# Performance work log

Hardware: AMD Instinct MI355X
Metric: run time of the kernel (lower is better)

Reference implementation:

```python
import jax, jax.numpy as jnp
import numpy as np
from jax import lax

B, T, V, E, H, K = 64, 512, 50002, 300, 256, 11
START, STOP = 9, 10


def _lstm_dir(x, w_ih, w_hh, b, reverse):
    """Single-direction LSTM. x: [B,T,D]; w_ih: [4H,D]; w_hh: [4H,H]; b: [4H]."""
    xw = jnp.einsum('btd,gd->btg', x, w_ih) + b  # precompute input projections [B,T,4H]
    h0 = jnp.zeros((x.shape[0], w_hh.shape[1]), x.dtype)

    def step(carry, xt):
        h, c = carry
        g = xt + h @ w_hh.T                      # [B,4H], gate order i,f,g,o (PyTorch)
        i, f, gg, o = jnp.split(g, 4, axis=-1)
        c = jax.nn.sigmoid(f) * c + jax.nn.sigmoid(i) * jnp.tanh(gg)
        h = jax.nn.sigmoid(o) * jnp.tanh(c)
        return (h, c), h

    _, hs = lax.scan(step, (h0, h0), jnp.swapaxes(xw, 0, 1), reverse=reverse)
    return jnp.swapaxes(hs, 0, 1)  # [B,T,H]


def _bilstm_feats(sentence, emb, fc_w, fc_b,
                  w_ih_l0f, w_hh_l0f, b_l0f, w_ih_l0b, w_hh_l0b, b_l0b,
                  w_ih_l1f, w_hh_l1f, b_l1f, w_ih_l1b, w_hh_l1b, b_l1b):
    x = emb[sentence]  # [B,T,E] (frozen embedding lookup)
    h0 = jnp.concatenate([
        _lstm_dir(x, w_ih_l0f, w_hh_l0f, b_l0f, False),
        _lstm_dir(x, w_ih_l0b, w_hh_l0b, b_l0b, True)], axis=-1)  # [B,T,2H]
    h1 = jnp.concatenate([
        _lstm_dir(h0, w_ih_l1f, w_hh_l1f, b_l1f, False),
        _lstm_dir(h0, w_ih_l1b, w_hh_l1b, b_l1b, True)], axis=-1)  # [B,T,2H]
    return h1 @ fc_w.T + fc_b  # emission scores [B,T,K] (dropout = identity in eval)


def _viterbi(feats, transitions):
    """feats: [B,T,K]; transitions[to, from]: [K,K]. Returns (path_score [B,1], path [B,T])."""
    Bs = feats.shape[0]
    init = jnp.full((Bs, K), -1000.0, feats.dtype).at[:, START].set(0.0)

    def step(fv, feat_t):
        scores = fv[:, None, :] + transitions[None, :, :]  # [B, next, prev]
        best_prev = jnp.argmax(scores, axis=2)             # [B,K]
        vit = jnp.max(scores, axis=2)                      # [B,K]
        return vit + feat_t, best_prev

    fv, bptrs = lax.scan(step, init, jnp.swapaxes(feats, 0, 1))  # bptrs: [T,B,K]
    terminal = fv + transitions[STOP]                             # [B,K]
    path_score = jnp.max(terminal, axis=1, keepdims=True)         # [B,1]
    last_tag = jnp.argmax(terminal, axis=1)                       # [B]

    def back(tag, bp):
        prev = jnp.take_along_axis(bp, tag[:, None], axis=1)[:, 0]
        return prev, prev

    _, prev_tags = lax.scan(back, last_tag, bptrs, reverse=True)  # prev_tags[t] = tag at t-1
    path = jnp.concatenate([prev_tags[1:], last_tag[None]], axis=0)  # [T,B]; drop START
    return path_score, jnp.swapaxes(path, 0, 1)


def setup_inputs() -> dict:
    key = jax.random.key(0)
    ks = jax.random.split(key, 24)
    s = 1.0 / np.sqrt(H)
    inp = {
        'sentence': jax.random.randint(ks[0], (B, T), 0, V, dtype=jnp.int32),
        'batch_lengths': jnp.full((B,), T, dtype=jnp.int32),
        'emb': jax.random.normal(ks[1], (V, E), jnp.float32) * 0.1,
        'fc_w': jax.random.normal(ks[2], (K, 2 * H), jnp.float32) * s,
        'fc_b': jnp.zeros((K,), jnp.float32),
    }
    trans = jax.random.normal(ks[3], (K, K), jnp.float32)
    inp['transitions'] = trans.at[START, :].set(-100000.0).at[:, STOP].set(-100000.0)
    i = 4
    for layer, din in ((0, E), (1, 2 * H)):
        for d in ('f', 'b'):
            inp[f'w_ih_l{layer}{d}'] = jax.random.normal(ks[i], (4 * H, din), jnp.float32) * s
            inp[f'w_hh_l{layer}{d}'] = jax.random.normal(ks[i + 1], (4 * H, H), jnp.float32) * s
            inp[f'b_l{layer}{d}'] = jax.random.normal(ks[i + 2], (4 * H,), jnp.float32) * s
            i += 3
    return inp


def reference(sentence, batch_lengths, emb, fc_w, fc_b, transitions,
              w_ih_l0f, w_hh_l0f, b_l0f, w_ih_l0b, w_hh_l0b, b_l0b,
              w_ih_l1f, w_hh_l1f, b_l1f, w_ih_l1b, w_hh_l1b, b_l1b):
    feats = _bilstm_feats(sentence, emb, fc_w, fc_b,
                          w_ih_l0f, w_hh_l0f, b_l0f, w_ih_l0b, w_hh_l0b, b_l0b,
                          w_ih_l1f, w_hh_l1f, b_l1f, w_ih_l1b, w_hh_l1b, b_l1b)
    score, path = _viterbi(feats, transitions)
    return score, path
```

## Files before the change

kernel.cpp:

```cpp
#include <hip/hip_runtime.h>
#include <cstddef>
#include <cstdint>
#include <math.h>


__device__ __forceinline__ float sigmf_(float x){ return 1.0f/(1.0f+expf(-x)); }

__global__ void k_zero(float* __restrict__ p, int n){
  for (int i = blockIdx.x*blockDim.x + threadIdx.x; i < n; i += gridDim.x*blockDim.x) p[i] = 0.f;
}

__global__ void k_gather(const int* __restrict__ sent, const float* __restrict__ emb,
                         float4* __restrict__ X, int b0, int t0, int logT, int Tm1, int total){
  int idx = blockIdx.x*256 + threadIdx.x;
  if (idx >= total) return;
  int m = idx / 76, k4 = idx - m*76;
  int bl = m >> logT, t = m & Tm1;
  float4 v = make_float4(0.f,0.f,0.f,0.f);
  if (k4 < 75) v = ((const float4*)emb)[(size_t)sent[(size_t)(b0+bl)*512 + t0 + t]*75 + k4];
  X[idx] = v;
}

__global__ void k_prepw(const float* __restrict__ w, float* __restrict__ wT, int din, int dinPad){
  int total = dinPad*1024;
  for (int idx = blockIdx.x*blockDim.x + threadIdx.x; idx < total; idx += gridDim.x*blockDim.x){
    int k = idx >> 10, n = idx & 1023;
    wT[idx] = (k < din) ? w[n*din + k] : 0.f;
  }
}

__global__ __launch_bounds__(256) void k_gemm2(
    const float* __restrict__ A0, const float* __restrict__ A1, int lda, int kTiles,
    int aBstride, int sOff0, int sOff1, int logT, int Tm1,
    const float* __restrict__ B0, const float* __restrict__ B1,
    const float* __restrict__ bias0, const float* __restrict__ bias1,
    float* __restrict__ C0, float* __restrict__ C1){
  __shared__ float As[16][132];
  __shared__ float Bs[16][132];
  const int z = blockIdx.z;
  const float* A   = z ? A1 : A0;
  const float* Bm  = z ? B1 : B0;
  const float* bias= z ? bias1 : bias0;
  float* Cc        = z ? C1 : C0;
  const int sOff   = z ? sOff1 : sOff0;
  const int t  = threadIdx.x;
  const int tx = t & 15, ty = t >> 4;
  const int m0 = blockIdx.y * 128, n0 = blockIdx.x * 128;
  const int arow = t >> 2, ak = (t & 3) * 4;
  const int brow = t >> 5, bc = (t & 31) * 4;
  const int gm0 = m0 + arow, gm1 = m0 + arow + 64;
  const size_t r0 = (size_t)(gm0 >> logT)*aBstride + sOff + (gm0 & Tm1);
  const size_t r1 = (size_t)(gm1 >> logT)*aBstride + sOff + (gm1 & Tm1);
  float acc[8][8] = {};
  for (int kt = 0; kt < kTiles; ++kt){
    const int kb = kt * 16;
    float4 a0 = *(const float4*)(A + r0*lda + kb + ak);
    float4 a1 = *(const float4*)(A + r1*lda + kb + ak);
    float4 b0 = *(const float4*)(Bm + (size_t)(kb+brow)*1024 + n0 + bc);
    float4 b1 = *(const float4*)(Bm + (size_t)(kb+brow+8)*1024 + n0 + bc);
    __syncthreads();
    As[ak+0][arow] = a0.x; As[ak+1][arow] = a0.y; As[ak+2][arow] = a0.z; As[ak+3][arow] = a0.w;
    As[ak+0][arow+64] = a1.x; As[ak+1][arow+64] = a1.y; As[ak+2][arow+64] = a1.z; As[ak+3][arow+64] = a1.w;
    *(float4*)&Bs[brow  ][bc] = b0;
    *(float4*)&Bs[brow+8][bc] = b1;
    __syncthreads();
    #pragma unroll
    for (int k = 0; k < 16; ++k){
      float av[8], bv[8];
      *(float4*)&av[0] = *(const float4*)&As[k][ty*8];
      *(float4*)&av[4] = *(const float4*)&As[k][ty*8+4];
      *(float4*)&bv[0] = *(const float4*)&Bs[k][tx*8];
      *(float4*)&bv[4] = *(const float4*)&Bs[k][tx*8+4];
      #pragma unroll
      for (int i = 0; i < 8; ++i)
        #pragma unroll
        for (int jj = 0; jj < 8; ++jj)
          acc[i][jj] = fmaf(av[i], bv[jj], acc[i][jj]);
    }
  }
  float bvals[8];
  *(float4*)&bvals[0] = *(const float4*)(bias + n0 + tx*8);
  *(float4*)&bvals[4] = *(const float4*)(bias + n0 + tx*8 + 4);
  float* Cp = Cc + (size_t)(m0 + ty*8)*1024 + n0 + tx*8;
  #pragma unroll
  for (int i = 0; i < 8; ++i){
    float4 o0 = make_float4(acc[i][0]+bvals[0], acc[i][1]+bvals[1], acc[i][2]+bvals[2], acc[i][3]+bvals[3]);
    float4 o1 = make_float4(acc[i][4]+bvals[4], acc[i][5]+bvals[5], acc[i][6]+bvals[6], acc[i][7]+bvals[7]);
    *(float4*)(Cp + (size_t)i*1024)     = o0;
    *(float4*)(Cp + (size_t)i*1024 + 4) = o1;
  }
}

__global__ __launch_bounds__(512) __attribute__((amdgpu_waves_per_eu(2, 2)))
void k_lstm2s(
    const float* __restrict__ xwF, const float* __restrict__ xwB,
    const float* __restrict__ whhf, const float* __restrict__ whhb,
    float* __restrict__ hout, int hBstride, int tOffF, int tOffB,
    int T, int epoch,
    float* __restrict__ hx, int* __restrict__ flags,
    float* __restrict__ hsave, float* __restrict__ csave)
{
  __shared__ float hfull[256];
  __shared__ float gls[512];
  __shared__ float wtail[512*66];
  const int blk = blockIdx.x;
  const int hh = (blk >> 3) & 1;
  const int chain = (blk & 7) | ((blk >> 4) << 3);
  const int b_local = chain >> 1;
  const int dir = chain & 1;
  const int t = threadIdx.x;
  const int gateK = t >> 7, i0 = t & 127;
  float4 wL[24], wR[24];
  {
    const float* whh = dir ? whhb : whhf;
    const float* base = whh + (size_t)(gateK*256 + hh*128 + i0)*256;
    const float* a = base + hh*128;
    const float* b = base + (1-hh)*128;
    #pragma unroll
    for (int q = 0; q < 24; ++q){ wL[q] = *(const float4*)(a + q*4); wR[q] = *(const float4*)(b + q*4); }
    for (int q = 24; q < 32; ++q){
      #pragma unroll
      for (int e = 0; e < 4; ++e){
        wtail[t*66 + (q-24)*4 + e]      = a[q*4 + e];
        wtail[t*66 + 32 + (q-24)*4 + e] = b[q*4 + e];
      }
    }
  }
  if (t < 256) hfull[t] = hsave[chain*256 + t];
  float c = (t < 128) ? csave[chain*256 + hh*128 + t] : 0.f;
  __syncthreads();
  const int xcol = gateK*256 + hh*128 + i0;
  const float* xb = (dir ? xwB : xwF) + (size_t)b_local*T*1024 + xcol;
  float* hxme        = hx + (size_t)(chain*2 + hh)*256;
  const float* hxpt  = hx + (size_t)(chain*2 + (1-hh))*256;
  int* flg  = flags + (chain*2 + hh)*16;
  int* flgp = flags + (chain*2 + (1-hh))*16;
  const int tOff = dir ? tOffB : tOffF;
  float* hob = hout + (size_t)b_local*hBstride + dir*256 + hh*128;
  const float* wtb = &wtail[t*66];
  const float4* hL4 = ((const float4*)hfull) + hh*32;
  const float4* hR4 = ((const float4*)hfull) + (1-hh)*32;
  float xg = xb[(size_t)(dir ? (T-1) : 0)*1024];
  float2 hrem = make_float2(0.f, 0.f);
  for (int s = 0; s < T; ++s){
    const int tt = dir ? (T-1-s) : s;
    float xn = 0.f;
    if (s < T-1) xn = xb[(size_t)(dir ? (T-2-s) : (s+1))*1024];
    if (s > 0 && t < 64){
      hfull[(1-hh)*128 + 2*t]     = hrem.x;
      hfull[(1-hh)*128 + 2*t + 1] = hrem.y;
    }
    float pa = 0.f;
    #pragma unroll
    for (int q = 0; q < 24; ++q){
      float4 hv = hL4[q];
      pa = fmaf(wL[q].x, hv.x, pa);
      pa = fmaf(wL[q].y, hv.y, pa);
      pa = fmaf(wL[q].z, hv.z, pa);
      pa = fmaf(wL[q].w, hv.w, pa);
    }
    #pragma unroll
    for (int q = 24; q < 32; ++q){
      float4 hv = hL4[q];
      const int o = (q-24)*4;
      pa = fmaf(wtb[o+0], hv.x, pa);
      pa = fmaf(wtb[o+1], hv.y, pa);
      pa = fmaf(wtb[o+2], hv.z, pa);
      pa = fmaf(wtb[o+3], hv.w, pa);
    }
    __syncthreads();
    float pb = 0.f;
    #pragma unroll
    for (int q = 0; q < 24; ++q){
      float4 hv = hR4[q];
      pb = fmaf(wR[q].x, hv.x, pb);
      pb = fmaf(wR[q].y, hv.y, pb);
      pb = fmaf(wR[q].z, hv.z, pb);
      pb = fmaf(wR[q].w, hv.w, pb);
    }
    #pragma unroll
    for (int q = 24; q < 32; ++q){
      float4 hv = hR4[q];
      const int o = (q-24)*4;
      pb = fmaf(wtb[32+o+0], hv.x, pb);
      pb = fmaf(wtb[32+o+1], hv.y, pb);
      pb = fmaf(wtb[32+o+2], hv.z, pb);
      pb = fmaf(wtb[32+o+3], hv.w, pb);
    }
    float acc = (pa + pb) + xg;
    float act = (gateK == 2) ? tanhf(acc) : sigmf_(acc);
    gls[t] = act;
    __syncthreads();
    float hval = 0.f;
    if (t < 128){
      c = gls[128 + t]*c + gls[t]*gls[256 + t];
      hval = gls[384 + t]*tanhf(c);
      hfull[hh*128 + t] = hval;
      __hip_atomic_store(&hxme[(s & 1)*128 + t], hval,
                         __ATOMIC_RELAXED, __HIP_MEMORY_SCOPE_AGENT);
    }
    __syncthreads();
    if (t == 0)
      __hip_atomic_store(flg, epoch + s + 1, __ATOMIC_RELAXED, __HIP_MEMORY_SCOPE_AGENT);
    if (t < 128) hob[(size_t)(tOff + tt)*512 + t] = hval;
    if (s < T-1){
      if (t == 0){
        int lim = 0;
        while (__hip_atomic_load(flgp, __ATOMIC_RELAXED, __HIP_MEMORY_SCOPE_AGENT) < epoch + s + 1
               && ++lim < (1<<20)) {}
      }
      if (t < 64){
        union { unsigned long long u; float2 f; } uu;
        uu.u = __hip_atomic_load((const unsigned long long*)(hxpt + (s & 1)*128 + 2*t),
                                 __ATOMIC_RELAXED, __HIP_MEMORY_SCOPE_AGENT);
        hrem = uu.f;
      }
    }
    xg = xn;
  }
  if (t < 128){
    hsave[chain*256 + hh*128 + t] = hfull[hh*128 + t];
    csave[chain*256 + hh*128 + t] = c;
  }
}

__global__ __launch_bounds__(256) void k_feats_half(
    const float* __restrict__ h1s, const float* __restrict__ fcw, const float* __restrict__ fcb,
    float* __restrict__ feats, int b0, int logT, int Tm1, int tG0, int dir){
  int wv = threadIdx.x >> 6, lane = threadIdx.x & 63;
  int m = blockIdx.x*4 + wv;
  const float4* row = (const float4*)(h1s + (size_t)m*512 + dir*256);
  float4 rv = row[lane];
  int bl = m >> logT, tl = m & Tm1;
  size_t fbase = ((size_t)(b0 + bl)*512 + tG0 + tl)*11;
  #pragma unroll
  for (int n = 0; n < 11; ++n){
    const float4* wr = (const float4*)(fcw + n*512 + dir*256);
    float4 w4 = wr[lane];
    float p = rv.x*w4.x + rv.y*w4.y + rv.z*w4.z + rv.w*w4.w;
    #pragma unroll
    for (int off = 32; off > 0; off >>= 1) p += __shfl_down(p, off, 64);
    if (lane == 0){
      float add = (dir == 0) ? (p + fcb[n]) : p;
      feats[fbase + n] += add;
    }
  }
}

__global__ __launch_bounds__(256) void k_viterbi(const float* __restrict__ feats,
                        const float* __restrict__ trans, float* __restrict__ out){
  __shared__ unsigned char bp[4][512][12];
  const int wave = threadIdx.x >> 6, lane = threadIdx.x & 63;
  const int b = blockIdx.x*4 + wave;
  const int j = lane;
  float tr[11];
  float fv;
  if (j < 11){
    #pragma unroll
    for (int p = 0; p < 11; ++p) tr[p] = trans[j*11 + p];
    fv = (j == 9) ? 0.f : -1000.f;
  } else {
    #pragma unroll
    for (int p = 0; p < 11; ++p) tr[p] = -1e30f;
    fv = -1e30f;
  }
  const float* fb = feats + ((size_t)b*512)*11 + j;
  float f0 = (j < 11) ? fb[0*11] : 0.f;
  float f1 = (j < 11) ? fb[1*11] : 0.f;
  float f2 = (j < 11) ? fb[2*11] : 0.f;
  float f3 = (j < 11) ? fb[3*11] : 0.f;
#define VSTEP(TT, FREG) {                                            \
    float best = -1e38f; int bestp = 0;                              \
    _Pragma("unroll")                                                \
    for (int p = 0; p < 11; ++p){                                    \
      float v = __shfl(fv, p, 64) + tr[p];                           \
      if (v > best){ best = v; bestp = p; }                          \
    }                                                                \
    fv = best + FREG;                                                \
    if (j < 11) bp[wave][TT][j] = (unsigned char)bestp; }
  for (int t = 0; t < 512; t += 4){
    VSTEP(t+0, f0); f0 = (j < 11 && t+4 < 512) ? fb[(size_t)(t+4)*11] : 0.f;
    VSTEP(t+1, f1); f1 = (j < 11 && t+5 < 512) ? fb[(size_t)(t+5)*11] : 0.f;
    VSTEP(t+2, f2); f2 = (j < 11 && t+6 < 512) ? fb[(size_t)(t+6)*11] : 0.f;
    VSTEP(t+3, f3); f3 = (j < 11 && t+7 < 512) ? fb[(size_t)(t+7)*11] : 0.f;
  }
#undef VSTEP
  float term = (j < 11) ? fv + trans[10*11 + j] : -1e38f;
  float best = -1e38f; int bestp = 0;
  #pragma unroll
  for (int p = 0; p < 11; ++p){
    float v = __shfl(term, p, 64);
    if (v > best){ best = v; bestp = p; }
  }
  if (lane == 0){
    out[b] = best;
    float* path = out + 64 + (size_t)b*512;
    int cur = bestp;
    path[511] = (float)cur;
    for (int t = 511; t >= 1; --t){
      cur = bp[wave][t][cur];
      path[t-1] = (float)cur;
    }
  }
}

extern "C" void kernel_launch(void* const* d_in, const int* in_sizes, int n_in,
                              void* d_out, int out_size, void* d_ws, size_t ws_size,
                              hipStream_t stream){
  const int*   sent  = (const int*)d_in[0];
  const float* emb   = (const float*)d_in[2];
  const float* fcw   = (const float*)d_in[3];
  const float* fcb   = (const float*)d_in[4];
  const float* trans = (const float*)d_in[5];
  const float* wih0f = (const float*)d_in[6];
  const float* whh0f = (const float*)d_in[7];
  const float* b0f   = (const float*)d_in[8];
  const float* wih0b = (const float*)d_in[9];
  const float* whh0b = (const float*)d_in[10];
  const float* b0b   = (const float*)d_in[11];
  const float* wih1f = (const float*)d_in[12];
  const float* whh1f = (const float*)d_in[13];
  const float* b1f   = (const float*)d_in[14];
  const float* wih1b = (const float*)d_in[15];
  const float* whh1b = (const float*)d_in[16];
  const float* b1b   = (const float*)d_in[17];

  float* ws = (float*)d_ws;
  const size_t o_wT0f = 0;
  const size_t o_wT0b = o_wT0f + 311296;
  const size_t o_wT1f = o_wT0b + 311296;
  const size_t o_wT1b = o_wT1f + 524288;
  const size_t o_hx   = o_wT1b + 524288;
  const size_t o_flag = o_hx   + 65536;
  const size_t o_hs   = o_flag + 4096;
  const size_t o_cs   = o_hs   + 32768;
  const size_t o_feat = o_cs   + 32768;
  const size_t o_var  = o_feat + 360448;
  float* wT0f = ws + o_wT0f;
  float* wT0b = ws + o_wT0b;
  float* wT1f = ws + o_wT1f;
  float* wT1b = ws + o_wT1b;
  float* hx    = ws + o_hx;
  int*   flags = (int*)(ws + o_flag);
  float* hsave = ws + o_hs;
  float* csave = ws + o_cs;
  float* feats = ws + o_feat;

  int C = 8, T = 32, logT = 5;
  {
    const int cc[9]  = {64, 64, 64, 32, 32, 16, 16, 8, 8};
    const int tt[9]  = {64, 32, 16, 32, 16, 32, 16, 64, 32};
    const int lt[9]  = { 6,  5,  4,  5,  4,  5,  4,  6,  5};
    for (int i = 0; i < 9; ++i){
      size_t need = (o_var + (size_t)cc[i]*tt[i]*2656 + (size_t)cc[i]*262144)*4;
      if (need <= ws_size){ C = cc[i]; T = tt[i]; logT = lt[i]; break; }
    }
  }
  const int Tm1 = T - 1, S = 512 / T;
  float* XF  = ws + o_var;
  float* XB  = XF + (size_t)C*T*304;
  float* xwF = XB + (size_t)C*T*304;
  float* xwB = xwF + (size_t)C*T*1024;
  float* h0  = xwB + (size_t)C*T*1024;
  float* h1s = XF;

  hipLaunchKernelGGL(k_prepw, dim3(512), dim3(256), 0, stream, wih0f, wT0f, 300, 304);
  hipLaunchKernelGGL(k_prepw, dim3(512), dim3(256), 0, stream, wih0b, wT0b, 300, 304);
  hipLaunchKernelGGL(k_prepw, dim3(512), dim3(256), 0, stream, wih1f, wT1f, 512, 512);
  hipLaunchKernelGGL(k_prepw, dim3(512), dim3(256), 0, stream, wih1b, wT1b, 512, 512);
  hipLaunchKernelGGL(k_zero,  dim3(512), dim3(256), 0, stream, feats, 360448);

  for (int b0 = 0; b0 < 64; b0 += C){
    for (int layer = 0; layer < 2; ++layer){
      hipLaunchKernelGGL(k_zero, dim3(256), dim3(256), 0, stream, ws + o_hx, 65536 + 4096 + 65536);
      const float* whF = layer ? whh1f : whh0f;
      const float* whB = layer ? whh1b : whh0b;
      for (int sl = 0; sl < S; ++sl){
        const int sF = sl, sB = S - 1 - sl;
        const int M = C*T;
        if (layer == 0){
          int total = C*T*76;
          hipLaunchKernelGGL(k_gather, dim3((total+255)/256), dim3(256), 0, stream,
                             sent, emb, (float4*)XF, b0, sF*T, logT, Tm1, total);
          hipLaunchKernelGGL(k_gather, dim3((total+255)/256), dim3(256), 0, stream,
                             sent, emb, (float4*)XB, b0, sB*T, logT, Tm1, total);
          hipLaunchKernelGGL(k_gemm2, dim3(8, M/128, 2), dim3(256), 0, stream,
                             XF, XB, 304, 19, T, 0, 0, logT, Tm1,
                             wT0f, wT0b, b0f, b0b, xwF, xwB);
        } else {
          hipLaunchKernelGGL(k_gemm2, dim3(8, M/128, 2), dim3(256), 0, stream,
                             h0, h0, 512, 32, 512, sF*T, sB*T, logT, Tm1,
                             wT1f, wT1b, b1f, b1b, xwF, xwB);
        }
        {
          const float *xF = xwF, *xB = xwB, *wF = whF, *wB = whB;
          float* hop = layer ? h1s : h0;
          int hBs  = layer ? T*512 : 512*512;
          int tOF  = layer ? 0 : sF*T;
          int tOB  = layer ? 0 : sB*T;
          int Tk = T, ep = sl*T;
          float *hxp = hx, *hsp = hsave, *csp = csave; int *flp = flags;
          void* args[] = {(void*)&xF, (void*)&xB, (void*)&wF, (void*)&wB,
                          (void*)&hop, (void*)&hBs, (void*)&tOF, (void*)&tOB,
                          (void*)&Tk, (void*)&ep,
                          (void*)&hxp, (void*)&flp, (void*)&hsp, (void*)&csp};
          hipLaunchCooperativeKernel((const void*)k_lstm2s, dim3(C*4), dim3(512), args, 0, stream);
        }
        if (layer == 1){
          hipLaunchKernelGGL(k_feats_half, dim3(C*T/4), dim3(256), 0, stream,
                             h1s, fcw, fcb, feats, b0, logT, Tm1, sF*T, 0);
          hipLaunchKernelGGL(k_feats_half, dim3(C*T/4), dim3(256), 0, stream,
                             h1s, fcw, fcb, feats, b0, logT, Tm1, sB*T, 1);
        }
      }
    }
  }
  hipLaunchKernelGGL(k_viterbi, dim3(16), dim3(256), 0, stream, feats, trans, (float*)d_out);
}
```

Baseline: 5.635 ms.

## Pack epoch tags with h values and move gate combine to wave shuffles

```diff
diff --git a/kernel.cpp b/kernel.cpp
--- a/kernel.cpp
+++ b/kernel.cpp
@@ -5,6 +5,13 @@
 
 
 __device__ __forceinline__ float sigmf_(float x){ return 1.0f/(1.0f+expf(-x)); }
+
+__device__ __forceinline__ void bar_sync(){
+  __builtin_amdgcn_sched_barrier(0);
+  asm volatile("s_waitcnt lgkmcnt(0)" ::: "memory");
+  __builtin_amdgcn_s_barrier();
+  __builtin_amdgcn_sched_barrier(0);
+}
 
 __global__ void k_zero(float* __restrict__ p, int n){
   for (int i = blockIdx.x*blockDim.x + threadIdx.x; i < n; i += gridDim.x*blockDim.x) p[i] = 0.f;
@@ -97,11 +104,10 @@
     const float* __restrict__ whhf, const float* __restrict__ whhb,
     float* __restrict__ hout, int hBstride, int tOffF, int tOffB,
     int T, int epoch,
-    float* __restrict__ hx, int* __restrict__ flags,
+    unsigned long long* __restrict__ hx,
     float* __restrict__ hsave, float* __restrict__ csave)
 {
   __shared__ float hfull[256];
-  __shared__ float gls[512];
   __shared__ float wtail[512*66];
   const int blk = blockIdx.x;
   const int hh = (blk >> 3) & 1;
@@ -109,7 +115,9 @@
   const int b_local = chain >> 1;
   const int dir = chain & 1;
   const int t = threadIdx.x;
-  const int gateK = t >> 7, i0 = t & 127;
+  const int w = t >> 6, l = t & 63;
+  const int gateK = l >> 4;
+  const int i0 = w*16 + (l & 15);
   float4 wL[24], wR[24];
   {
     const float* whh = dir ? whhb : whhf;
@@ -127,29 +135,23 @@
     }
   }
   if (t < 256) hfull[t] = hsave[chain*256 + t];
-  float c = (t < 128) ? csave[chain*256 + hh*128 + t] : 0.f;
+  float c = (l < 16) ? csave[chain*256 + hh*128 + i0] : 0.f;
   __syncthreads();
   const int xcol = gateK*256 + hh*128 + i0;
   const float* xb = (dir ? xwB : xwF) + (size_t)b_local*T*1024 + xcol;
-  float* hxme        = hx + (size_t)(chain*2 + hh)*256;
-  const float* hxpt  = hx + (size_t)(chain*2 + (1-hh))*256;
-  int* flg  = flags + (chain*2 + hh)*16;
-  int* flgp = flags + (chain*2 + (1-hh))*16;
+  unsigned long long* hxme       = hx + (size_t)(chain*2 + hh)*256;
+  const unsigned long long* hxpt = hx + (size_t)(chain*2 + (1-hh))*256;
   const int tOff = dir ? tOffB : tOffF;
   float* hob = hout + (size_t)b_local*hBstride + dir*256 + hh*128;
   const float* wtb = &wtail[t*66];
   const float4* hL4 = ((const float4*)hfull) + hh*32;
   const float4* hR4 = ((const float4*)hfull) + (1-hh)*32;
   float xg = xb[(size_t)(dir ? (T-1) : 0)*1024];
-  float2 hrem = make_float2(0.f, 0.f);
+  float hlast = 0.f;
   for (int s = 0; s < T; ++s){
     const int tt = dir ? (T-1-s) : s;
     float xn = 0.f;
     if (s < T-1) xn = xb[(size_t)(dir ? (T-2-s) : (s+1))*1024];
-    if (s > 0 && t < 64){
-      hfull[(1-hh)*128 + 2*t]     = hrem.x;
-      hfull[(1-hh)*128 + 2*t + 1] = hrem.y;
-    }
     float pa = 0.f;
     #pragma unroll
     for (int q = 0; q < 24; ++q){
@@ -168,7 +170,22 @@
       pa = fmaf(wtb[o+2], hv.z, pa);
       pa = fmaf(wtb[o+3], hv.w, pa);
     }
-    __syncthreads();
+    if (s > 0 && w == 0){
+      const unsigned long long* src = hxpt + (size_t)(((s-1)&1))*128;
+      const unsigned want = (unsigned)(epoch + s);
+      unsigned long long v0 = 0, v1 = 0;
+      bool ok0 = false, ok1 = false;
+      int lim = 0;
+      do {
+        if (!ok0){ v0 = __hip_atomic_load(src + 2*l,     __ATOMIC_RELAXED, __HIP_MEMORY_SCOPE_AGENT);
+                   ok0 = (unsigned)(v0 >> 32) == want; }
+        if (!ok1){ v1 = __hip_atomic_load(src + 2*l + 1, __ATOMIC_RELAXED, __HIP_MEMORY_SCOPE_AGENT);
+                   ok1 = (unsigned)(v1 >> 32) == want; }
+      } while (__any(!(ok0 && ok1)) && ++lim < (1<<20));
+      hfull[(1-hh)*128 + 2*l]     = __uint_as_float((unsigned)v0);
+      hfull[(1-hh)*128 + 2*l + 1] = __uint_as_float((unsigned)v1);
+    }
+    bar_sync();
     float pb = 0.f;
     #pragma unroll
     for (int q = 0; q < 24; ++q){
@@ -189,38 +206,26 @@
     }
     float acc = (pa + pb) + xg;
     float act = (gateK == 2) ? tanhf(acc) : sigmf_(acc);
-    gls[t] = act;
-    __syncthreads();
-    float hval = 0.f;
-    if (t < 128){
-      c = gls[128 + t]*c + gls[t]*gls[256 + t];
-      hval = gls[384 + t]*tanhf(c);
-      hfull[hh*128 + t] = hval;
-      __hip_atomic_store(&hxme[(s & 1)*128 + t], hval,
+    float fg = __shfl(act, (l & 15) + 16, 64);
+    float gg = __shfl(act, (l & 15) + 32, 64);
+    float og = __shfl(act, (l & 15) + 48, 64);
+    if (l < 16){
+      c = fg*c + act*gg;
+      float hval = og*tanhf(c);
+      hlast = hval;
+      hfull[hh*128 + i0] = hval;
+      unsigned long long pk = ((unsigned long long)(unsigned)(epoch + s + 1) << 32)
+                            | (unsigned long long)__float_as_uint(hval);
+      __hip_atomic_store(&hxme[(size_t)(s & 1)*128 + i0], pk,
                          __ATOMIC_RELAXED, __HIP_MEMORY_SCOPE_AGENT);
-    }
-    __syncthreads();
-    if (t == 0)
-      __hip_atomic_store(flg, epoch + s + 1, __ATOMIC_RELAXED, __HIP_MEMORY_SCOPE_AGENT);
-    if (t < 128) hob[(size_t)(tOff + tt)*512 + t] = hval;
-    if (s < T-1){
-      if (t == 0){
-        int lim = 0;
-        while (__hip_atomic_load(flgp, __ATOMIC_RELAXED, __HIP_MEMORY_SCOPE_AGENT) < epoch + s + 1
-               && ++lim < (1<<20)) {}
-      }
-      if (t < 64){
-        union { unsigned long long u; float2 f; } uu;
-        uu.u = __hip_atomic_load((const unsigned long long*)(hxpt + (s & 1)*128 + 2*t),
-                                 __ATOMIC_RELAXED, __HIP_MEMORY_SCOPE_AGENT);
-        hrem = uu.f;
-      }
-    }
+      hob[(size_t)(tOff + tt)*512 + i0] = hval;
+    }
+    bar_sync();
     xg = xn;
   }
-  if (t < 128){
-    hsave[chain*256 + hh*128 + t] = hfull[hh*128 + t];
-    csave[chain*256 + hh*128 + t] = c;
+  if (l < 16){
+    hsave[chain*256 + hh*128 + i0] = hlast;
+    csave[chain*256 + hh*128 + i0] = c;
   }
 }
 
@@ -331,8 +336,7 @@
   const size_t o_wT1f = o_wT0b + 311296;
   const size_t o_wT1b = o_wT1f + 524288;
   const size_t o_hx   = o_wT1b + 524288;
-  const size_t o_flag = o_hx   + 65536;
-  const size_t o_hs   = o_flag + 4096;
+  const size_t o_hs   = o_hx   + 131072;
   const size_t o_cs   = o_hs   + 32768;
   const size_t o_feat = o_cs   + 32768;
   const size_t o_var  = o_feat + 360448;
@@ -340,18 +344,17 @@
   float* wT0b = ws + o_wT0b;
   float* wT1f = ws + o_wT1f;
   float* wT1b = ws + o_wT1b;
-  float* hx    = ws + o_hx;
-  int*   flags = (int*)(ws + o_flag);
+  unsigned long long* hx = (unsigned long long*)(ws + o_hx);
   float* hsave = ws + o_hs;
   float* csave = ws + o_cs;
   float* feats = ws + o_feat;
 
   int C = 8, T = 32, logT = 5;
   {
-    const int cc[9]  = {64, 64, 64, 32, 32, 16, 16, 8, 8};
-    const int tt[9]  = {64, 32, 16, 32, 16, 32, 16, 64, 32};
-    const int lt[9]  = { 6,  5,  4,  5,  4,  5,  4,  6,  5};
-    for (int i = 0; i < 9; ++i){
+    const int cc[12] = {64, 64, 64, 64, 64, 32, 32, 16, 16, 8, 8, 8};
+    const int tt[12] = {512,256,128, 64, 32, 32, 16, 32, 16, 64, 32, 16};
+    const int lt[12] = {  9,  8,  7,  6,  5,  5,  4,  5,  4,  6,  5, 4};
+    for (int i = 0; i < 12; ++i){
       size_t need = (o_var + (size_t)cc[i]*tt[i]*2656 + (size_t)cc[i]*262144)*4;
       if (need <= ws_size){ C = cc[i]; T = tt[i]; logT = lt[i]; break; }
     }
@@ -372,7 +375,7 @@
 
   for (int b0 = 0; b0 < 64; b0 += C){
     for (int layer = 0; layer < 2; ++layer){
-      hipLaunchKernelGGL(k_zero, dim3(256), dim3(256), 0, stream, ws + o_hx, 65536 + 4096 + 65536);
+      hipLaunchKernelGGL(k_zero, dim3(256), dim3(256), 0, stream, ws + o_hx, 131072 + 32768 + 32768);
       const float* whF = layer ? whh1f : whh0f;
       const float* whB = layer ? whh1b : whh0b;
       for (int sl = 0; sl < S; ++sl){
@@ -399,11 +402,12 @@
           int tOF  = layer ? 0 : sF*T;
           int tOB  = layer ? 0 : sB*T;
           int Tk = T, ep = sl*T;
-          float *hxp = hx, *hsp = hsave, *csp = csave; int *flp = flags;
+          unsigned long long* hxp = hx;
+          float *hsp = hsave, *csp = csave;
           void* args[] = {(void*)&xF, (void*)&xB, (void*)&wF, (void*)&wB,
                           (void*)&hop, (void*)&hBs, (void*)&tOF, (void*)&tOB,
                           (void*)&Tk, (void*)&ep,
-                          (void*)&hxp, (void*)&flp, (void*)&hsp, (void*)&csp};
+                          (void*)&hxp, (void*)&hsp, (void*)&csp};
           hipLaunchCooperativeKernel((const void*)k_lstm2s, dim3(C*4), dim3(512), args, 0, stream);
         }
         if (layer == 1){
```

Result: slower. 15.50 ms (+175.2%).
